# Kernel optimization log

Hardware: AMD Instinct MI355X
Metric: run time of the kernel (lower is better)

Reference implementation:

```python
import jax, jax.numpy as jnp
import numpy as np

EMBED_DIM = 1024
NUM_HEADS = 16
HEAD_DIM = EMBED_DIM // NUM_HEADS
NEG = -1000000000.0


def setup_inputs() -> dict:
    key = jax.random.key(0)
    ks = jax.random.split(key, 13)
    B, S, D = 4, 2048, EMBED_DIM
    scale = 1.0 / np.sqrt(D)
    inp = {
        "query": jax.random.normal(ks[0], (B, S, D), jnp.float32),
        "key": jax.random.normal(ks[1], (B, S, D), jnp.float32),
        "value": jax.random.normal(ks[2], (B, S, D), jnp.float32),
        "mask": jax.random.randint(ks[3], (B, 1, 1, S), 0, 2, jnp.int32),
        "Wq": jax.random.normal(ks[4], (D, D), jnp.float32) * scale,
        "bq": jnp.zeros((D,), jnp.float32),
        "Wk": jax.random.normal(ks[5], (D, D), jnp.float32) * scale,
        "bk": jnp.zeros((D,), jnp.float32),
        "Wv": jax.random.normal(ks[6], (D, D), jnp.float32) * scale,
        "bv": jnp.zeros((D,), jnp.float32),
        "Wo": jax.random.normal(ks[7], (D, D), jnp.float32) * scale,
        "bo": jnp.zeros((D,), jnp.float32),
    }
    return inp


def _split_heads(x):
    B, S, D = x.shape
    return x.reshape(B, S, NUM_HEADS, HEAD_DIM).transpose(0, 2, 1, 3)  # [B,H,S,hd]


def reference(query, key, value, mask, Wq, bq, Wk, bk, Wv, bv, Wo, bo):
    B, S, D = query.shape
    Q = _split_heads(query @ Wq + bq)
    K = _split_heads(key @ Wk + bk)
    V = _split_heads(value @ Wv + bv)
    scores = jnp.einsum("bhqd,bhkd->bhqk", Q, K) / jnp.sqrt(jnp.float32(HEAD_DIM))
    scores = jnp.where(mask == 0, jnp.float32(NEG), scores)
    attn = jax.nn.softmax(scores, axis=-1)
    out = jnp.einsum("bhqk,bhkd->bhqd", attn, V)
    out = out.transpose(0, 2, 1, 3).reshape(B, S, D)
    return out @ Wo + bo
```

## Files before the change

### kernel.cpp

```cpp
#include <hip/hip_runtime.h>


#define SEQ   2048
#define EDIM  1024
#define NHEAD 16
#define HDIM  64
#define NBAT  4
#define MTOK  8192

typedef __attribute__((ext_vector_type(8))) __bf16 bf16x8;
typedef __attribute__((ext_vector_type(4))) __bf16 bf16x4;
typedef __attribute__((ext_vector_type(4))) float f32x4;
typedef __attribute__((ext_vector_type(16))) float f32x16;
typedef __attribute__((ext_vector_type(8))) unsigned short us8;
typedef unsigned short u16;

#define SCL   0.1803368801111244f

__device__ __forceinline__ u16 bfbits(float f) {
    __bf16 h = (__bf16)f;
    return __builtin_bit_cast(u16, h);
}
__device__ __forceinline__ bf16x8 bc(us8 v) { return __builtin_bit_cast(bf16x8, v); }
__device__ __forceinline__ float exp2fast(float x) {
    float r;
    asm("v_exp_f32 %0, %1" : "=v"(r) : "v"(x));
    return r;
}
__device__ __forceinline__ void glds16(const void* g, void* l) {
    __builtin_amdgcn_global_load_lds(
        (const __attribute__((address_space(1))) unsigned int*)g,
        (__attribute__((address_space(3))) unsigned int*)l, 16, 0, 0);
}

__global__ __launch_bounds__(256) void prep_kernel(const int* __restrict__ mask,
                                                   int* __restrict__ idxl,
                                                   int* __restrict__ cntp) {
    __shared__ int psum[257];
    const int b = blockIdx.x, t = threadIdx.x;
    const int* mp = mask + b * SEQ;
    int m8[8]; int s = 0;
#pragma unroll
    for (int i = 0; i < 8; ++i) { m8[i] = mp[t * 8 + i]; s += (m8[i] != 0); }
    psum[t + 1] = s;
    __syncthreads();
    if (t == 0) { psum[0] = 0; for (int i = 1; i <= 256; ++i) psum[i] += psum[i - 1]; }
    __syncthreads();
    int ex = psum[t];
#pragma unroll
    for (int i = 0; i < 8; ++i)
        if (m8[i] != 0) idxl[b * SEQ + (ex++)] = t * 8 + i;
    if (t == 0) cntp[b] = psum[256];
}

__global__ __launch_bounds__(256) void wtrans4_kernel(const float* __restrict__ W0,
                                                      const float* __restrict__ W1,
                                                      const float* __restrict__ W2,
                                                      const float* __restrict__ W3,
                                                      u16* __restrict__ WT) {
    __shared__ float tile[32][33];
    const int tx = threadIdx.x, ty = threadIdx.y;
    const int bx = blockIdx.x,  by = blockIdx.y, wz = blockIdx.z;
    const float* W = (wz == 0) ? W0 : (wz == 1) ? W1 : (wz == 2) ? W2 : W3;
    u16* O = WT + (size_t)wz * EDIM * EDIM;
#pragma unroll
    for (int i = 0; i < 4; ++i)
        tile[ty + i * 8][tx] = W[(size_t)(by * 32 + ty + i * 8) * EDIM + bx * 32 + tx];
    __syncthreads();
#pragma unroll
    for (int i = 0; i < 4; ++i) {
        int n = bx * 32 + ty + i * 8;
        int k = by * 32 + tx;
        O[(size_t)n * EDIM + k] = bfbits(tile[tx][ty + i * 8]);
    }
}

template <int MODE, bool AFP32, bool GATHER>
__global__ __launch_bounds__(256) void gemm_kernel(const void* __restrict__ Ap,
                                                   const u16* __restrict__ WT,
                                                   const float* __restrict__ bias,
                                                   void* __restrict__ outp,
                                                   const int* __restrict__ idxl,
                                                   const int* __restrict__ cntp,
                                                   const float oscale) {
    const int bm = blockIdx.x, bn = blockIdx.y;
    int cn = 0;
    if constexpr (GATHER) {
        cn = cntp[bm >> 4];
        if (((bm & 15) * 128) >= cn) return;
    }

    __shared__ __align__(16) char Asraw[2][128 * 32 * (AFP32 ? 4 : 2)];
    __shared__ __align__(16) u16 Bs[2][128][32];

    const int tid  = threadIdx.x;
    const int lane = tid & 63, w = tid >> 6;
    const int g    = lane >> 4, l15 = lane & 15;
    const int wrow = w >> 1, wcol = w & 1;

    const char* pa[4];
    if constexpr (AFP32) {
        const float* A = (const float*)Ap;
#pragma unroll
        for (int t = 0; t < 4; ++t) {
            const int rloc = w * 32 + t * 8 + (lane >> 3);
            int arow;
            if constexpr (GATHER) {
                const int sloc = (bm & 15) * 128 + rloc;
                const int gi = (sloc < cn) ? idxl[(bm >> 4) * SEQ + sloc] : 0;
                arow = (bm >> 4) * SEQ + gi;
            } else arow = bm * 128 + rloc;
            const int scol = ((lane & 7) ^ (lane >> 3)) * 4;
            pa[t] = (const char*)(A + (size_t)arow * EDIM + scol);
        }
    } else {
        const u16* A = (const u16*)Ap;
#pragma unroll
        for (int t = 0; t < 2; ++t) {
            const int rloc = w * 32 + t * 16 + (lane >> 2);
            const int arow = bm * 128 + rloc;
            const int scol = ((lane & 3) ^ ((lane >> 3) & 3)) * 8;
            pa[t] = (const char*)(A + (size_t)arow * EDIM + scol);
        }
    }
    const char* pb[2];
#pragma unroll
    for (int t = 0; t < 2; ++t) {
        const int rloc = w * 32 + t * 16 + (lane >> 2);
        const int brow = bn * 128 + rloc;
        const int scol = ((lane & 3) ^ ((lane >> 3) & 3)) * 8;
        pb[t] = (const char*)(WT + (size_t)brow * EDIM + scol);
    }

    auto STAGE = [&](int buf, int ko) {
        char* abase = &Asraw[buf][0] + w * (AFP32 ? 4096 : 2048);
        if constexpr (AFP32) {
#pragma unroll
            for (int t = 0; t < 4; ++t)
                glds16(pa[t] + (size_t)ko * 4, abase + t * 1024);
        } else {
#pragma unroll
            for (int t = 0; t < 2; ++t)
                glds16(pa[t] + (size_t)ko * 2, abase + t * 1024);
        }
        char* bbase = (char*)&Bs[buf][0][0] + w * 2048;
#pragma unroll
        for (int t = 0; t < 2; ++t)
            glds16(pb[t] + (size_t)ko * 2, bbase + t * 1024);
    };

    f32x4 acc[4][4] = {};

    STAGE(0, 0);
    __syncthreads();

    int buf = 0;
#pragma unroll 1
    for (int kt = 0; kt < EDIM / 32; ++kt) {
        if (kt < EDIM / 32 - 1) STAGE(buf ^ 1, (kt + 1) * 32);

        bf16x8 af[4], bfr[4];
        if constexpr (AFP32) {
            const float* As = (const float*)&Asraw[buf][0];
            const int x = l15 & 7;
#pragma unroll
            for (int i = 0; i < 4; ++i) {
                const int row = wrow * 64 + i * 16 + l15;
                f32x4 u0 = *(const f32x4*)(As + row * 32 + (((2 * g)     ^ x) * 4));
                f32x4 u1 = *(const f32x4*)(As + row * 32 + (((2 * g + 1) ^ x) * 4));
#pragma unroll
                for (int j = 0; j < 4; ++j) {
                    af[i][j]     = (__bf16)u0[j];
                    af[i][4 + j] = (__bf16)u1[j];
                }
            }
        } else {
            const u16* As = (const u16*)&Asraw[buf][0];
            const int x = (l15 >> 1) & 3;
#pragma unroll
            for (int i = 0; i < 4; ++i) {
                const int row = wrow * 64 + i * 16 + l15;
                af[i] = bc(*(const us8*)(As + row * 32 + ((g ^ x) * 8)));
            }
        }
        {
            const int x = (l15 >> 1) & 3;
#pragma unroll
            for (int j = 0; j < 4; ++j) {
                const int row = wcol * 64 + j * 16 + l15;
                bfr[j] = bc(*(const us8*)((const u16*)&Bs[buf][0][0] + row * 32 + ((g ^ x) * 8)));
            }
        }

#pragma unroll
        for (int i = 0; i < 4; ++i)
#pragma unroll
            for (int j = 0; j < 4; ++j)
                acc[i][j] = __builtin_amdgcn_mfma_f32_16x16x32_bf16(af[i], bfr[j], acc[i][j], 0, 0, 0);

        __syncthreads();
        buf ^= 1;
    }

#pragma unroll
    for (int i = 0; i < 4; ++i) {
#pragma unroll
        for (int j = 0; j < 4; ++j) {
            const int gm0 = bm * 128 + wrow * 64 + i * 16 + g * 4;
            const int gn  = bn * 128 + wcol * 64 + j * 16 + l15;
            const float bv = bias[gn];
#pragma unroll
            for (int r = 0; r < 4; ++r) {
                float val = (acc[i][j][r] + bv) * oscale;
                const int m = gm0 + r;
                if constexpr (GATHER) {
                    if ((m & 2047) >= cn) val = 0.f;
                }
                if constexpr (MODE == 2) {
                    ((float*)outp)[(size_t)m * EDIM + gn] = val;
                } else {
                    const int b = m >> 11, s = m & 2047;
                    const int h = gn >> 6, d = gn & 63;
                    u16* O = (u16*)outp;
                    if constexpr (MODE == 0)
                        O[((size_t)(b * NHEAD + h) << 17) + s * HDIM + d] = bfbits(val);
                    else
                        O[((size_t)(b * NHEAD + h) << 17) + d * SEQ + s] = bfbits(val);
                }
            }
        }
    }
}

__global__ __launch_bounds__(256) void attn_kernel(const u16* __restrict__ Q,
                                                   const u16* __restrict__ K,
                                                   const u16* __restrict__ VT,
                                                   const int* __restrict__ cntp,
                                                   u16* __restrict__ O) {
    __shared__ u16 Klds[2][64][64];
    __shared__ u16 Vlds[2][64][64];

    const int tid = threadIdx.x, lane = tid & 63, w = tid >> 6;
    const int h = lane >> 5, l31 = lane & 31;

    const int id  = blockIdx.x;
    const int bh  = (id & 7) * 8 + ((id >> 3) >> 4);
    const int qb  = (id >> 3) & 15;
    const int b   = bh >> 4, hd_ = bh & 15;

    const u16* Qp = Q + ((size_t)bh << 17);
    const u16* Kp = K + ((size_t)bh << 17);
    const u16* Vp = VT + ((size_t)bh << 17);
    const int q0w = qb * 128 + w * 32;

    const int cn  = cntp[b];
    const int ktc = (cn + 63) >> 6;

    bf16x8 qf[4];
#pragma unroll
    for (int khd = 0; khd < 4; ++khd)
        qf[khd] = bc(*(const us8*)&Qp[(size_t)(q0w + l31) * HDIM + khd * 16 + h * 8]);

    const int b_  = l31 & 3, hp = (l31 >> 2) & 1, cc = l31 >> 3;
    const int piR = 16 * (cc & 1) + 8 * hp + 4 * (cc >> 1) + b_;
    const int swk = (piR & 3) ^ (((piR >> 3) & 3) << 1);
    const int swv = l31 & 7;

    const int lr = lane >> 3, lg = lane & 7;
    const u16* pKs[2]; const u16* pVs[2];
#pragma unroll
    for (int t = 0; t < 2; ++t) {
        const int rloc = w * 16 + t * 8 + lr;
        const int xk = (rloc & 3) ^ (((rloc >> 3) & 3) << 1);
        pKs[t] = Kp + (size_t)rloc * HDIM + ((lg ^ xk) << 3);
        const int xv = rloc & 7;
        pVs[t] = Vp + (size_t)rloc * SEQ + ((lg ^ xv) << 3);
    }

    auto STAGE = [&](int bufn, int kb) {
#pragma unroll
        for (int t = 0; t < 2; ++t) {
            glds16(pKs[t] + (size_t)kb * HDIM, &Klds[bufn][w * 16 + t * 8][0]);
            glds16(pVs[t] + kb,                &Vlds[bufn][w * 16 + t * 8][0]);
        }
    };

    f32x16 ot[2] = {};
    f32x16 ls = {};

    bf16x8 onesf;
#pragma unroll
    for (int j = 0; j < 8; ++j) onesf[j] = (__bf16)1.0f;

    STAGE(0, 0);
    __syncthreads();

    for (int kt = 0; kt < ktc; ++kt) {
        const int cur = kt & 1;
        const bool more = (kt + 1) < ktc;
        if (more) STAGE(cur ^ 1, (kt + 1) * 64);

        f32x16 st[2] = {};
        __builtin_amdgcn_s_setprio(1);
#pragma unroll
        for (int kb2 = 0; kb2 < 2; ++kb2) {
            const u16* Kr = &Klds[cur][kb2 * 32 + piR][0];
#pragma unroll
            for (int khd = 0; khd < 4; ++khd) {
                bf16x8 kf = bc(*(const us8*)&Kr[(khd * 16 + h * 8) ^ (swk << 3)]);
                st[kb2] = __builtin_amdgcn_mfma_f32_32x32x16_bf16(kf, qf[khd], st[kb2], 0, 0, 0);
            }
        }
        __builtin_amdgcn_s_setprio(0);

#pragma unroll
        for (int kb2 = 0; kb2 < 2; ++kb2)
#pragma unroll
            for (int e = 0; e < 16; ++e)
                st[kb2][e] = exp2fast(st[kb2][e]);

        if (kt == ktc - 1) {
            const int kbase = kt * 64;
#pragma unroll
            for (int kb2 = 0; kb2 < 2; ++kb2)
#pragma unroll
                for (int cp = 0; cp < 4; ++cp)
#pragma unroll
                    for (int j = 0; j < 4; ++j) {
                        const int key = kbase + kb2 * 32 + 16 * (cp & 1) + 4 * (cp >> 1) + 8 * h + j;
                        if (key >= cn) st[kb2][cp * 4 + j] = 0.f;
                    }
        }

        bf16x8 pf[4];
#pragma unroll
        for (int s = 0; s < 4; ++s) {
            const int kb2 = s >> 1, sel = (s & 1) * 4;
#pragma unroll
            for (int j = 0; j < 4; ++j) {
                pf[s][j]     = (__bf16)st[kb2][sel + j];
                pf[s][4 + j] = (__bf16)st[kb2][8 + sel + j];
            }
        }

        __builtin_amdgcn_s_setprio(1);
#pragma unroll
        for (int s = 0; s < 4; ++s)
            ls = __builtin_amdgcn_mfma_f32_32x32x16_bf16(onesf, pf[s], ls, 0, 0, 0);
#pragma unroll
        for (int dblk = 0; dblk < 2; ++dblk) {
            const u16* Vr = &Vlds[cur][dblk * 32 + l31][0];
#pragma unroll
            for (int s = 0; s < 4; ++s) {
                bf16x8 vf = bc(*(const us8*)&Vr[(s * 16 + h * 8) ^ (swv << 3)]);
                ot[dblk] = __builtin_amdgcn_mfma_f32_32x32x16_bf16(vf, pf[s], ot[dblk], 0, 0, 0);
            }
        }
        __builtin_amdgcn_s_setprio(0);

        __syncthreads();
    }

    const float inv = 1.f / ls[0];

    const size_t row = (size_t)(b * SEQ + q0w + l31) * EDIM + hd_ * HDIM;
#pragma unroll
    for (int dblk = 0; dblk < 2; ++dblk) {
#pragma unroll
        for (int cp = 0; cp < 4; ++cp) {
            bf16x4 t;
#pragma unroll
            for (int j = 0; j < 4; ++j)
                t[j] = (__bf16)(ot[dblk][cp * 4 + j] * inv);
            *(bf16x4*)&O[row + dblk * 32 + 8 * cp + 4 * h] = t;
        }
    }
}

extern "C" void kernel_launch(void* const* d_in, const int* in_sizes, int n_in,
                              void* d_out, int out_size, void* d_ws, size_t ws_size,
                              hipStream_t stream) {
    const float* query = (const float*)d_in[0];
    const float* key   = (const float*)d_in[1];
    const float* value = (const float*)d_in[2];
    const int*   mask  = (const int*)d_in[3];
    const float* Wq = (const float*)d_in[4];  const float* bq = (const float*)d_in[5];
    const float* Wk = (const float*)d_in[6];  const float* bk = (const float*)d_in[7];
    const float* Wv = (const float*)d_in[8];  const float* bv = (const float*)d_in[9];
    const float* Wo = (const float*)d_in[10]; const float* bo = (const float*)d_in[11];

    char* ws = (char*)d_ws;
    const size_t WT_BYTES  = (size_t)EDIM * EDIM * 2;
    const size_t BUF_BYTES = (size_t)MTOK * EDIM * 2;
    u16* wtq   = (u16*)(ws);
    u16* wtk   = (u16*)(ws + WT_BYTES);
    u16* wtv   = (u16*)(ws + 2 * WT_BYTES);
    u16* wto   = (u16*)(ws + 3 * WT_BYTES);
    u16* Qbuf  = (u16*)(ws + 4 * WT_BYTES);
    u16* Kbuf  = (u16*)(ws + 4 * WT_BYTES + BUF_BYTES);
    u16* VTbuf = (u16*)(ws + 4 * WT_BYTES + 2 * BUF_BYTES);
    u16* Abuf  = (u16*)(ws + 4 * WT_BYTES + 3 * BUF_BYTES);
    int* idxl  = (int*)(ws + 4 * WT_BYTES + 4 * BUF_BYTES);
    int* cntp  = (int*)(ws + 4 * WT_BYTES + 4 * BUF_BYTES + (size_t)MTOK * 4);

    prep_kernel<<<NBAT, 256, 0, stream>>>(mask, idxl, cntp);

    dim3 tgrid(32, 32, 4), tblk(32, 8);
    wtrans4_kernel<<<tgrid, tblk, 0, stream>>>(Wq, Wk, Wv, Wo, wtq);

    dim3 ggrid(MTOK / 128, EDIM / 128);
    gemm_kernel<0, true,  false><<<ggrid, 256, 0, stream>>>(query, wtq, bq, Qbuf, nullptr, nullptr, 1.0f);
    gemm_kernel<0, true,  true ><<<ggrid, 256, 0, stream>>>(key,   wtk, bk, Kbuf, idxl, cntp, SCL);
    gemm_kernel<1, true,  true ><<<ggrid, 256, 0, stream>>>(value, wtv, bv, VTbuf, idxl, cntp, 1.0f);

    attn_kernel<<<1024, 256, 0, stream>>>(Qbuf, Kbuf, VTbuf, cntp, Abuf);

    gemm_kernel<2, false, false><<<ggrid, 256, 0, stream>>>(Abuf, wto, bo, (float*)d_out, nullptr, nullptr, 1.0f);
}
```

Baseline: 196.0 us.

## Triple-buffer GEMM and attention LDS staging with partial vmcnt waits

Both the projection GEMM and the attention kernel move from double to triple buffering of their LDS tiles, prefetching two tiles ahead. The full __syncthreads waits are replaced by s_waitcnt vmcnt(N) plus a raw s_barrier, so loads for the next-next tile stay in flight while the current tile is consumed. This aims to hide global-to-LDS latency better, at the cost of more LDS per block (possible occupancy loss) and reliance on hand-counted outstanding-load numbers being correct.

```diff
diff --git a/kernel.cpp b/kernel.cpp
--- a/kernel.cpp
+++ b/kernel.cpp
@@ -32,6 +32,7 @@
         (const __attribute__((address_space(1))) unsigned int*)g,
         (__attribute__((address_space(3))) unsigned int*)l, 16, 0, 0);
 }
+#define VMCNT(n) asm volatile("s_waitcnt vmcnt(" #n ")" ::: "memory")
 
 __global__ __launch_bounds__(256) void prep_kernel(const int* __restrict__ mask,
                                                    int* __restrict__ idxl,
@@ -90,8 +91,9 @@
         if (((bm & 15) * 128) >= cn) return;
     }
 
-    __shared__ __align__(16) char Asraw[2][128 * 32 * (AFP32 ? 4 : 2)];
-    __shared__ __align__(16) u16 Bs[2][128][32];
+    constexpr int ASZ = 128 * 32 * (AFP32 ? 4 : 2);
+    __shared__ __align__(16) char Asraw[3][ASZ];
+    __shared__ __align__(16) u16 Bs[3][128][32];
 
     const int tid  = threadIdx.x;
     const int lane = tid & 63, w = tid >> 6;
@@ -132,8 +134,8 @@
         pb[t] = (const char*)(WT + (size_t)brow * EDIM + scol);
     }
 
-    auto STAGE = [&](int buf, int ko) {
-        char* abase = &Asraw[buf][0] + w * (AFP32 ? 4096 : 2048);
+    auto STAGE = [&](int bufn, int ko) {
+        char* abase = &Asraw[bufn][0] + w * (AFP32 ? 4096 : 2048);
         if constexpr (AFP32) {
 #pragma unroll
             for (int t = 0; t < 4; ++t)
@@ -143,25 +145,28 @@
             for (int t = 0; t < 2; ++t)
                 glds16(pa[t] + (size_t)ko * 2, abase + t * 1024);
         }
-        char* bbase = (char*)&Bs[buf][0][0] + w * 2048;
+        char* bbase = (char*)&Bs[bufn][0][0] + w * 2048;
 #pragma unroll
         for (int t = 0; t < 2; ++t)
             glds16(pb[t] + (size_t)ko * 2, bbase + t * 1024);
     };
 
     f32x4 acc[4][4] = {};
+    constexpr int NT = EDIM / 32;
 
     STAGE(0, 0);
-    __syncthreads();
-
-    int buf = 0;
+    STAGE(1, 32);
+    if constexpr (AFP32) VMCNT(6); else VMCNT(4);
+    __builtin_amdgcn_s_barrier();
+
+    int bcur = 0, bn1 = 1, bn2 = 2;
 #pragma unroll 1
-    for (int kt = 0; kt < EDIM / 32; ++kt) {
-        if (kt < EDIM / 32 - 1) STAGE(buf ^ 1, (kt + 1) * 32);
+    for (int kt = 0; kt < NT; ++kt) {
+        if (kt + 2 < NT) STAGE(bn2, (kt + 2) * 32);
 
         bf16x8 af[4], bfr[4];
         if constexpr (AFP32) {
-            const float* As = (const float*)&Asraw[buf][0];
+            const float* As = (const float*)&Asraw[bcur][0];
             const int x = l15 & 7;
 #pragma unroll
             for (int i = 0; i < 4; ++i) {
@@ -175,7 +180,7 @@
                 }
             }
         } else {
-            const u16* As = (const u16*)&Asraw[buf][0];
+            const u16* As = (const u16*)&Asraw[bcur][0];
             const int x = (l15 >> 1) & 3;
 #pragma unroll
             for (int i = 0; i < 4; ++i) {
@@ -188,7 +193,7 @@
 #pragma unroll
             for (int j = 0; j < 4; ++j) {
                 const int row = wcol * 64 + j * 16 + l15;
-                bfr[j] = bc(*(const us8*)((const u16*)&Bs[buf][0][0] + row * 32 + ((g ^ x) * 8)));
+                bfr[j] = bc(*(const us8*)((const u16*)&Bs[bcur][0][0] + row * 32 + ((g ^ x) * 8)));
             }
         }
 
@@ -198,8 +203,15 @@
             for (int j = 0; j < 4; ++j)
                 acc[i][j] = __builtin_amdgcn_mfma_f32_16x16x32_bf16(af[i], bfr[j], acc[i][j], 0, 0, 0);
 
-        __syncthreads();
-        buf ^= 1;
+        if (kt + 1 < NT) {
+            if (kt + 2 < NT) {
+                if constexpr (AFP32) VMCNT(6); else VMCNT(4);
+            } else {
+                VMCNT(0);
+            }
+            __builtin_amdgcn_s_barrier();
+        }
+        const int t = bcur; bcur = bn1; bn1 = bn2; bn2 = t;
     }
 
 #pragma unroll
@@ -237,8 +249,8 @@
                                                    const u16* __restrict__ VT,
                                                    const int* __restrict__ cntp,
                                                    u16* __restrict__ O) {
-    __shared__ u16 Klds[2][64][64];
-    __shared__ u16 Vlds[2][64][64];
+    __shared__ u16 Klds[3][64][64];
+    __shared__ u16 Vlds[3][64][64];
 
     const int tid = threadIdx.x, lane = tid & 63, w = tid >> 6;
     const int h = lane >> 5, l31 = lane & 31;
@@ -293,18 +305,18 @@
     for (int j = 0; j < 8; ++j) onesf[j] = (__bf16)1.0f;
 
     STAGE(0, 0);
-    __syncthreads();
-
+    if (ktc > 1) { STAGE(1, 64); VMCNT(4); } else { VMCNT(0); }
+    __builtin_amdgcn_s_barrier();
+
+    int bcur = 0, bn1 = 1, bn2 = 2;
     for (int kt = 0; kt < ktc; ++kt) {
-        const int cur = kt & 1;
-        const bool more = (kt + 1) < ktc;
-        if (more) STAGE(cur ^ 1, (kt + 1) * 64);
+        if (kt + 2 < ktc) STAGE(bn2, (kt + 2) * 64);
 
         f32x16 st[2] = {};
         __builtin_amdgcn_s_setprio(1);
 #pragma unroll
         for (int kb2 = 0; kb2 < 2; ++kb2) {
-            const u16* Kr = &Klds[cur][kb2 * 32 + piR][0];
+            const u16* Kr = &Klds[bcur][kb2 * 32 + piR][0];
 #pragma unroll
             for (int khd = 0; khd < 4; ++khd) {
                 bf16x8 kf = bc(*(const us8*)&Kr[(khd * 16 + h * 8) ^ (swk << 3)]);
@@ -349,7 +361,7 @@
             ls = __builtin_amdgcn_mfma_f32_32x32x16_bf16(onesf, pf[s], ls, 0, 0, 0);
 #pragma unroll
         for (int dblk = 0; dblk < 2; ++dblk) {
-            const u16* Vr = &Vlds[cur][dblk * 32 + l31][0];
+            const u16* Vr = &Vlds[bcur][dblk * 32 + l31][0];
 #pragma unroll
             for (int s = 0; s < 4; ++s) {
                 bf16x8 vf = bc(*(const us8*)&Vr[(s * 16 + h * 8) ^ (swv << 3)]);
@@ -358,7 +370,11 @@
         }
         __builtin_amdgcn_s_setprio(0);
 
-        __syncthreads();
+        if (kt + 1 < ktc) {
+            if (kt + 2 < ktc) { VMCNT(4); } else { VMCNT(0); }
+            __builtin_amdgcn_s_barrier();
+        }
+        const int t = bcur; bcur = bn1; bn1 = bn2; bn2 = t;
     }
 
     const float inv = 1.f / ls[0];
```

Measured after the change: 198.3 us. Within noise of the previous version (+1.2%).

## Fuse Q/K/V projection GEMMs into one launch with tile-swizzled block order

Applied to the files above, without the earlier changes.

Merges the three separate Q, K and V projection GEMM launches into a single 1536-block kernel that picks its input, weight, bias and output layout by block index. Both it and a dedicated output-projection GEMM remap block ids so groups of M-tiles sharing an N-tile run together, aiming for better L2 reuse of weight tiles. It also changes the K LDS swizzle pattern in attention to reduce bank conflicts. The cost is runtime branching on `which` instead of compile-time templates, which may raise register use slightly.

```diff
diff --git a/kernel.cpp b/kernel.cpp
--- a/kernel.cpp
+++ b/kernel.cpp
@@ -75,23 +75,36 @@
     }
 }
 
-template <int MODE, bool AFP32, bool GATHER>
-__global__ __launch_bounds__(256) void gemm_kernel(const void* __restrict__ Ap,
-                                                   const u16* __restrict__ WT,
-                                                   const float* __restrict__ bias,
-                                                   void* __restrict__ outp,
-                                                   const int* __restrict__ idxl,
-                                                   const int* __restrict__ cntp,
-                                                   const float oscale) {
-    const int bm = blockIdx.x, bn = blockIdx.y;
-    int cn = 0;
-    if constexpr (GATHER) {
+__global__ __launch_bounds__(256) void qkv_gemm_kernel(
+        const float* __restrict__ Aq, const float* __restrict__ Ak,
+        const float* __restrict__ Av, const u16* __restrict__ WTall,
+        const float* __restrict__ bqp, const float* __restrict__ bkp,
+        const float* __restrict__ bvp,
+        u16* __restrict__ Qb, u16* __restrict__ Kb, u16* __restrict__ Vb,
+        const int* __restrict__ idxl, const int* __restrict__ cntp) {
+    const int id    = blockIdx.x;
+    const int which = id >> 9;
+    const int sub   = id & 511;
+    const int r_    = sub >> 3;
+    const int grp   = r_ >> 5, bnq = (r_ >> 2) & 7, bmin = r_ & 3;
+    const int bm    = (sub & 7) + 8 * (grp * 4 + bmin);
+    const int bn    = bnq;
+
+    const float* A    = (which == 0) ? Aq : (which == 1) ? Ak : Av;
+    const u16*   WT   = WTall + (size_t)which * EDIM * EDIM;
+    const float* bias = (which == 0) ? bqp : (which == 1) ? bkp : bvp;
+    u16*         outp = (which == 0) ? Qb : (which == 1) ? Kb : Vb;
+    const float  oscale = (which == 1) ? SCL : 1.0f;
+    const bool   gather = (which > 0);
+
+    int cn = SEQ;
+    if (gather) {
         cn = cntp[bm >> 4];
         if (((bm & 15) * 128) >= cn) return;
     }
 
-    __shared__ __align__(16) char Asraw[2][128 * 32 * (AFP32 ? 4 : 2)];
-    __shared__ __align__(16) u16 Bs[2][128][32];
+    __shared__ __align__(16) float As[2][128 * 32];
+    __shared__ __align__(16) u16   Bs[2][128][32];
 
     const int tid  = threadIdx.x;
     const int lane = tid & 63, w = tid >> 6;
@@ -99,29 +112,17 @@
     const int wrow = w >> 1, wcol = w & 1;
 
     const char* pa[4];
-    if constexpr (AFP32) {
-        const float* A = (const float*)Ap;
-#pragma unroll
-        for (int t = 0; t < 4; ++t) {
-            const int rloc = w * 32 + t * 8 + (lane >> 3);
-            int arow;
-            if constexpr (GATHER) {
-                const int sloc = (bm & 15) * 128 + rloc;
-                const int gi = (sloc < cn) ? idxl[(bm >> 4) * SEQ + sloc] : 0;
-                arow = (bm >> 4) * SEQ + gi;
-            } else arow = bm * 128 + rloc;
-            const int scol = ((lane & 7) ^ (lane >> 3)) * 4;
-            pa[t] = (const char*)(A + (size_t)arow * EDIM + scol);
-        }
-    } else {
-        const u16* A = (const u16*)Ap;
-#pragma unroll
-        for (int t = 0; t < 2; ++t) {
-            const int rloc = w * 32 + t * 16 + (lane >> 2);
-            const int arow = bm * 128 + rloc;
-            const int scol = ((lane & 3) ^ ((lane >> 3) & 3)) * 8;
-            pa[t] = (const char*)(A + (size_t)arow * EDIM + scol);
-        }
+#pragma unroll
+    for (int t = 0; t < 4; ++t) {
+        const int rloc = w * 32 + t * 8 + (lane >> 3);
+        int arow;
+        if (gather) {
+            const int sloc = (bm & 15) * 128 + rloc;
+            const int gi = (sloc < cn) ? idxl[(bm >> 4) * SEQ + sloc] : 0;
+            arow = (bm >> 4) * SEQ + gi;
+        } else arow = bm * 128 + rloc;
+        const int scol = ((lane & 7) ^ (lane >> 3)) * 4;
+        pa[t] = (const char*)(A + (size_t)arow * EDIM + scol);
     }
     const char* pb[2];
 #pragma unroll
@@ -132,56 +133,43 @@
         pb[t] = (const char*)(WT + (size_t)brow * EDIM + scol);
     }
 
-    auto STAGE = [&](int buf, int ko) {
-        char* abase = &Asraw[buf][0] + w * (AFP32 ? 4096 : 2048);
-        if constexpr (AFP32) {
-#pragma unroll
-            for (int t = 0; t < 4; ++t)
-                glds16(pa[t] + (size_t)ko * 4, abase + t * 1024);
-        } else {
-#pragma unroll
-            for (int t = 0; t < 2; ++t)
-                glds16(pa[t] + (size_t)ko * 2, abase + t * 1024);
-        }
-        char* bbase = (char*)&Bs[buf][0][0] + w * 2048;
+    auto STAGE = [&](int bufn, int ko) {
+        char* abase = (char*)&As[bufn][0] + w * 4096;
+#pragma unroll
+        for (int t = 0; t < 4; ++t)
+            glds16(pa[t] + (size_t)ko * 4, abase + t * 1024);
+        char* bbase = (char*)&Bs[bufn][0][0] + w * 2048;
 #pragma unroll
         for (int t = 0; t < 2; ++t)
             glds16(pb[t] + (size_t)ko * 2, bbase + t * 1024);
     };
 
     f32x4 acc[4][4] = {};
+    constexpr int NT = EDIM / 32;
 
     STAGE(0, 0);
     __syncthreads();
 
     int buf = 0;
 #pragma unroll 1
-    for (int kt = 0; kt < EDIM / 32; ++kt) {
-        if (kt < EDIM / 32 - 1) STAGE(buf ^ 1, (kt + 1) * 32);
+    for (int kt = 0; kt < NT; ++kt) {
+        if (kt < NT - 1) STAGE(buf ^ 1, (kt + 1) * 32);
 
         bf16x8 af[4], bfr[4];
-        if constexpr (AFP32) {
-            const float* As = (const float*)&Asraw[buf][0];
+        {
+            const float* Ab = &As[buf][0];
             const int x = l15 & 7;
 #pragma unroll
             for (int i = 0; i < 4; ++i) {
                 const int row = wrow * 64 + i * 16 + l15;
-                f32x4 u0 = *(const f32x4*)(As + row * 32 + (((2 * g)     ^ x) * 4));
-                f32x4 u1 = *(const f32x4*)(As + row * 32 + (((2 * g + 1) ^ x) * 4));
+                f32x4 u0 = *(const f32x4*)(Ab + row * 32 + (((2 * g)     ^ x) * 4));
+                f32x4 u1 = *(const f32x4*)(Ab + row * 32 + (((2 * g + 1) ^ x) * 4));
 #pragma unroll
                 for (int j = 0; j < 4; ++j) {
                     af[i][j]     = (__bf16)u0[j];
                     af[i][4 + j] = (__bf16)u1[j];
                 }
             }
-        } else {
-            const u16* As = (const u16*)&Asraw[buf][0];
-            const int x = (l15 >> 1) & 3;
-#pragma unroll
-            for (int i = 0; i < 4; ++i) {
-                const int row = wrow * 64 + i * 16 + l15;
-                af[i] = bc(*(const us8*)(As + row * 32 + ((g ^ x) * 8)));
-            }
         }
         {
             const int x = (l15 >> 1) & 3;
@@ -213,21 +201,96 @@
             for (int r = 0; r < 4; ++r) {
                 float val = (acc[i][j][r] + bv) * oscale;
                 const int m = gm0 + r;
-                if constexpr (GATHER) {
-                    if ((m & 2047) >= cn) val = 0.f;
-                }
-                if constexpr (MODE == 2) {
-                    ((float*)outp)[(size_t)m * EDIM + gn] = val;
-                } else {
-                    const int b = m >> 11, s = m & 2047;
-                    const int h = gn >> 6, d = gn & 63;
-                    u16* O = (u16*)outp;
-                    if constexpr (MODE == 0)
-                        O[((size_t)(b * NHEAD + h) << 17) + s * HDIM + d] = bfbits(val);
-                    else
-                        O[((size_t)(b * NHEAD + h) << 17) + d * SEQ + s] = bfbits(val);
-                }
-            }
+                if (gather && (m & 2047) >= cn) val = 0.f;
+                const int b = m >> 11, s = m & 2047;
+                const int h = gn >> 6, d = gn & 63;
+                if (which == 2)
+                    outp[((size_t)(b * NHEAD + h) << 17) + d * SEQ + s] = bfbits(val);
+                else
+                    outp[((size_t)(b * NHEAD + h) << 17) + s * HDIM + d] = bfbits(val);
+            }
+        }
+    }
+}
+
+__global__ __launch_bounds__(256) void o_gemm_kernel(const u16* __restrict__ Ap,
+                                                     const u16* __restrict__ WT,
+                                                     const float* __restrict__ bias,
+                                                     float* __restrict__ outp) {
+    const int id  = blockIdx.x;
+    const int r_  = id >> 3;
+    const int grp = r_ >> 5, bnq = (r_ >> 2) & 7, bmin = r_ & 3;
+    const int bm  = (id & 7) + 8 * (grp * 4 + bmin);
+    const int bn  = bnq;
+
+    __shared__ __align__(16) u16 As[2][128][32];
+    __shared__ __align__(16) u16 Bs[2][128][32];
+
+    const int tid  = threadIdx.x;
+    const int lane = tid & 63, w = tid >> 6;
+    const int g    = lane >> 4, l15 = lane & 15;
+    const int wrow = w >> 1, wcol = w & 1;
+
+    const char* pa[2]; const char* pb[2];
+#pragma unroll
+    for (int t = 0; t < 2; ++t) {
+        const int rloc = w * 32 + t * 16 + (lane >> 2);
+        const int scol = ((lane & 3) ^ ((lane >> 3) & 3)) * 8;
+        pa[t] = (const char*)(Ap + (size_t)(bm * 128 + rloc) * EDIM + scol);
+        pb[t] = (const char*)(WT + (size_t)(bn * 128 + rloc) * EDIM + scol);
+    }
+
+    auto STAGE = [&](int bufn, int ko) {
+        char* abase = (char*)&As[bufn][0][0] + w * 2048;
+        char* bbase = (char*)&Bs[bufn][0][0] + w * 2048;
+#pragma unroll
+        for (int t = 0; t < 2; ++t) {
+            glds16(pa[t] + (size_t)ko * 2, abase + t * 1024);
+            glds16(pb[t] + (size_t)ko * 2, bbase + t * 1024);
+        }
+    };
+
+    f32x4 acc[4][4] = {};
+    constexpr int NT = EDIM / 32;
+
+    STAGE(0, 0);
+    __syncthreads();
+
+    int buf = 0;
+#pragma unroll 1
+    for (int kt = 0; kt < NT; ++kt) {
+        if (kt < NT - 1) STAGE(buf ^ 1, (kt + 1) * 32);
+
+        bf16x8 af[4], bfr[4];
+        const int x = (l15 >> 1) & 3;
+#pragma unroll
+        for (int i = 0; i < 4; ++i) {
+            const int rowA = wrow * 64 + i * 16 + l15;
+            af[i] = bc(*(const us8*)((const u16*)&As[buf][0][0] + rowA * 32 + ((g ^ x) * 8)));
+            const int rowB = wcol * 64 + i * 16 + l15;
+            bfr[i] = bc(*(const us8*)((const u16*)&Bs[buf][0][0] + rowB * 32 + ((g ^ x) * 8)));
+        }
+
+#pragma unroll
+        for (int i = 0; i < 4; ++i)
+#pragma unroll
+            for (int j = 0; j < 4; ++j)
+                acc[i][j] = __builtin_amdgcn_mfma_f32_16x16x32_bf16(af[i], bfr[j], acc[i][j], 0, 0, 0);
+
+        __syncthreads();
+        buf ^= 1;
+    }
+
+#pragma unroll
+    for (int i = 0; i < 4; ++i) {
+#pragma unroll
+        for (int j = 0; j < 4; ++j) {
+            const int gm0 = bm * 128 + wrow * 64 + i * 16 + g * 4;
+            const int gn  = bn * 128 + wcol * 64 + j * 16 + l15;
+            const float bv = bias[gn];
+#pragma unroll
+            for (int r = 0; r < 4; ++r)
+                outp[(size_t)(gm0 + r) * EDIM + gn] = acc[i][j][r] + bv;
         }
     }
 }
@@ -263,7 +326,7 @@
 
     const int b_  = l31 & 3, hp = (l31 >> 2) & 1, cc = l31 >> 3;
     const int piR = 16 * (cc & 1) + 8 * hp + 4 * (cc >> 1) + b_;
-    const int swk = (piR & 3) ^ (((piR >> 3) & 3) << 1);
+    const int swk = b_ | (hp << 2);
     const int swv = l31 & 7;
 
     const int lr = lane >> 3, lg = lane & 7;
@@ -271,7 +334,7 @@
 #pragma unroll
     for (int t = 0; t < 2; ++t) {
         const int rloc = w * 16 + t * 8 + lr;
-        const int xk = (rloc & 3) ^ (((rloc >> 3) & 3) << 1);
+        const int xk = (rloc & 3) | (((rloc >> 3) & 1) << 2);
         pKs[t] = Kp + (size_t)rloc * HDIM + ((lg ^ xk) << 3);
         const int xv = rloc & 7;
         pVs[t] = Vp + (size_t)rloc * SEQ + ((lg ^ xv) << 3);
@@ -393,8 +456,6 @@
     const size_t WT_BYTES  = (size_t)EDIM * EDIM * 2;
     const size_t BUF_BYTES = (size_t)MTOK * EDIM * 2;
     u16* wtq   = (u16*)(ws);
-    u16* wtk   = (u16*)(ws + WT_BYTES);
-    u16* wtv   = (u16*)(ws + 2 * WT_BYTES);
     u16* wto   = (u16*)(ws + 3 * WT_BYTES);
     u16* Qbuf  = (u16*)(ws + 4 * WT_BYTES);
     u16* Kbuf  = (u16*)(ws + 4 * WT_BYTES + BUF_BYTES);
@@ -408,12 +469,11 @@
     dim3 tgrid(32, 32, 4), tblk(32, 8);
     wtrans4_kernel<<<tgrid, tblk, 0, stream>>>(Wq, Wk, Wv, Wo, wtq);
 
-    dim3 ggrid(MTOK / 128, EDIM / 128);
-    gemm_kernel<0, true,  false><<<ggrid, 256, 0, stream>>>(query, wtq, bq, Qbuf, nullptr, nullptr, 1.0f);
-    gemm_kernel<0, true,  true ><<<ggrid, 256, 0, stream>>>(key,   wtk, bk, Kbuf, idxl, cntp, SCL);
-    gemm_kernel<1, true,  true ><<<ggrid, 256, 0, stream>>>(value, wtv, bv, VTbuf, idxl, cntp, 1.0f);
+    qkv_gemm_kernel<<<1536, 256, 0, stream>>>(query, key, value, wtq,
+                                              bq, bk, bv, Qbuf, Kbuf, VTbuf,
+                                              idxl, cntp);
 
     attn_kernel<<<1024, 256, 0, stream>>>(Qbuf, Kbuf, VTbuf, cntp, Abuf);
 
-    gemm_kernel<2, false, false><<<ggrid, 256, 0, stream>>>(Abuf, wto, bo, (float*)d_out, nullptr, nullptr, 1.0f);
-}
+    o_gemm_kernel<<<512, 256, 0, stream>>>(Abuf, wto, bo, (float*)d_out);
+}
```

Result: faster. 179.7 us (-8.3%).
